# Kernel optimization log

Measured on AMD Instinct MI355X. Metric: run time of the kernel, lower is better.

## Reference

```python
import jax, jax.numpy as jnp
import numpy as np

# Config from module init / global Args
H = 8        # n_head
DK = 64      # d_k
DV = 64      # d_v
D = 512      # d_model
KSZ = 3      # kernel_size (args.kernel_size)
B_PARAM = 0.001
CUR_HEAD = 3
ALPHA_C = -float(np.log(B_PARAM / (H - 1) * CUR_HEAD))  # alpha_c (nonzero head)
EPS = 1e-6


def setup_inputs() -> dict:
    key = jax.random.key(0)
    ks = jax.random.split(key, 8)
    B, L = 2, 2048
    q = jax.random.normal(ks[0], (B, L, D), jnp.float32)
    k = jax.random.normal(ks[1], (B, L, D), jnp.float32)
    v = jax.random.normal(ks[2], (B, L, D), jnp.float32)
    # Linear weights stored torch-style: [out_features, in_features]
    w_q = jax.random.normal(ks[3], (H * DK, D), jnp.float32) * 0.02
    w_k = jax.random.normal(ks[4], (H * DK, D), jnp.float32) * 0.02
    w_v = jax.random.normal(ks[5], (H * DV, D), jnp.float32) * 0.02
    w_fc = jax.random.normal(ks[6], (D, H * DV), jnp.float32) * 0.02
    gamma = jnp.ones((D,), jnp.float32)
    beta = jnp.zeros((D,), jnp.float32)
    return {"q": q, "k": k, "v": v, "w_q": w_q, "w_k": w_k, "w_v": w_v,
            "w_fc": w_fc, "gamma": gamma, "beta": beta}


def reference(q, k, v, w_q, w_k, w_v, w_fc, gamma, beta):
    B, L, _ = q.shape
    residual = q
    # QKV projections -> [B, H, L, d]
    qh = jnp.einsum('bld,ed->ble', q, w_q).reshape(B, L, H, DK).transpose(0, 2, 1, 3)
    kh = jnp.einsum('bld,ed->ble', k, w_k).reshape(B, L, H, DK).transpose(0, 2, 1, 3)
    vh = jnp.einsum('bld,ed->ble', v, w_v).reshape(B, L, H, DV).transpose(0, 2, 1, 3)
    # Scores: matmul(q / sqrt(d_k), k^T)  (LaSAttention receives d_k = d_k**0.5)
    attn = jnp.einsum('bhqd,bhkd->bhqk', qh, kh) / jnp.sqrt(jnp.float32(DK))
    # Distance weighting: eld = alpha_c * -(x - y) * attn, d_l[i,j] = j - i
    idx = jnp.arange(L)
    d_l = idx[None, :] - idx[:, None]                      # [L, L]
    eld_mat = (-ALPHA_C * d_l).astype(attn.dtype)
    eld = eld_mat[None, None, :, :] * attn
    # Softmax then avg_pool1d(kernel=KSZ, stride=1, pad=(KSZ-1)//2, count_include_pad)
    p = jax.nn.softmax(eld, axis=-1)                       # [B, H, L, L]
    pad = (KSZ - 1) // 2
    pp = jnp.pad(p, ((0, 0), (0, 0), (0, 0), (pad, pad)))
    pooled = sum(pp[..., j:j + L] for j in range(KSZ)) / jnp.float32(KSZ)
    # Value matmul (seq lengths equal so no trimming needed)
    out = jnp.einsum('bhqk,bhkd->bhqd', pooled, vh)
    out = out.transpose(0, 2, 1, 3).reshape(B, L, H * DV)
    # Output projection (dropout is identity in eval), residual, LayerNorm
    out = jnp.einsum('ble,de->bld', out, w_fc)
    out = out[:, :, None, :] + residual[:, :, None, :]     # [B, L, 1, D]
    mu = out.mean(axis=-1, keepdims=True)
    var = ((out - mu) ** 2).mean(axis=-1, keepdims=True)
    out = (out - mu) / jnp.sqrt(var + EPS) * gamma + beta
    return (out, pooled)
```

## Files before the change

kernel.cpp:

```cpp
#include <hip/hip_runtime.h>
#include <cstddef>
#include <cstdint>

#define ALPHA_C 7.7550531393693407f
constexpr int BB = 2;
constexpr int LL = 2048;
constexpr int HH = 8;
constexpr size_t OUT0  = (size_t)BB * LL * 512;
constexpr size_t PLANE = (size_t)BB * HH * LL * 64;
constexpr size_t XN    = (size_t)BB * LL * 512;
constexpr size_t WN    = (size_t)512 * 512;

typedef __attribute__((ext_vector_type(8))) short bf16x8;
typedef __attribute__((ext_vector_type(4))) short short4v;
typedef __attribute__((ext_vector_type(4))) float f32x4;

__device__ inline short f2bf(float x) {
  union { float f; unsigned u; } un; un.f = x;
  unsigned r = un.u + 0x7fffu + ((un.u >> 16) & 1u);
  return (short)(r >> 16);
}
__device__ inline float bf2f(short s) {
  union { unsigned u; float f; } un; un.u = ((unsigned)(unsigned short)s) << 16;
  return un.f;
}
__device__ inline void split3(float x, short& h, short& m, short& l) {
  h = f2bf(x); float r = x - bf2f(h);
  m = f2bf(r); float r2 = r - bf2f(m);
  l = f2bf(r2);
}

__global__ __launch_bounds__(256) void k_split3x(
    const float* __restrict__ a, const float* __restrict__ b, const float* __restrict__ c,
    short* __restrict__ da, short* __restrict__ db, short* __restrict__ dc, size_t n)
{
  size_t i = ((size_t)blockIdx.x * 256 + threadIdx.x) * 4;
  if (i >= n) return;
  const float* srcs[3] = {a, b, c};
  short* dsts[3] = {da, db, dc};
  #pragma unroll
  for (int s = 0; s < 3; ++s) {
    float4 x = *(const float4*)&srcs[s][i];
    short4v h, m, l;
    short th, tm, tl;
    split3(x.x, th, tm, tl); h[0] = th; m[0] = tm; l[0] = tl;
    split3(x.y, th, tm, tl); h[1] = th; m[1] = tm; l[1] = tl;
    split3(x.z, th, tm, tl); h[2] = th; m[2] = tm; l[2] = tl;
    split3(x.w, th, tm, tl); h[3] = th; m[3] = tm; l[3] = tl;
    *(short4v*)&dsts[s][i]         = h;
    *(short4v*)&dsts[s][n + i]     = m;
    *(short4v*)&dsts[s][2 * n + i] = l;
  }
}

__global__ __launch_bounds__(256) void k_cvtbf(
    const float* __restrict__ src, short* __restrict__ dst, size_t n)
{
  size_t i = ((size_t)blockIdx.x * 256 + threadIdx.x) * 8;
  if (i >= n) return;
  float4 a = *(const float4*)&src[i];
  float4 b = *(const float4*)&src[i + 4];
  bf16x8 o;
  o[0] = f2bf(a.x); o[1] = f2bf(a.y); o[2] = f2bf(a.z); o[3] = f2bf(a.w);
  o[4] = f2bf(b.x); o[5] = f2bf(b.y); o[6] = f2bf(b.z); o[7] = f2bf(b.w);
  *(bf16x8*)&dst[i] = o;
}

__global__ __launch_bounds__(256) void k_vavg(
    const short* __restrict__ vt, short* __restrict__ vavgt)
{
  const size_t row = blockIdx.x;
  const short* src = vt + row * LL;
  short* dst = vavgt + row * LL;
  const int c0 = threadIdx.x * 8;
  bf16x8 x = *(const bf16x8*)&src[c0];
  float xf[10];
  xf[0] = (c0 > 0) ? bf2f(src[c0 - 1]) : 0.f;
  #pragma unroll
  for (int i = 0; i < 8; ++i) xf[i + 1] = bf2f(x[i]);
  xf[9] = (c0 + 8 < LL) ? bf2f(src[c0 + 8]) : 0.f;
  bf16x8 o;
  #pragma unroll
  for (int i = 0; i < 8; ++i) o[i] = f2bf((xf[i] + xf[i + 1] + xf[i + 2]) * (1.0f / 3.0f));
  *(bf16x8*)&dst[c0] = o;
}

__global__ __launch_bounds__(256) void k_proj(
    const short* __restrict__ xq, const short* __restrict__ xk, const short* __restrict__ xv,
    const short* __restrict__ wq3, const short* __restrict__ wk3, const short* __restrict__ wv3,
    short* __restrict__ qs, short* __restrict__ ks, short* __restrict__ vt)
{
  const int bx  = blockIdx.x;
  const int sel = bx >> 3;
  const int n0  = (bx & 7) * 64;
  const int m0  = blockIdx.y * 64;
  const short* X = sel == 0 ? xq  : (sel == 1 ? xk  : xv);
  const short* W = sel == 0 ? wq3 : (sel == 1 ? wk3 : wv3);

  __shared__ short Xs[3][64 * 72];
  __shared__ short Ws[3][64 * 72];
  const int tid = threadIdx.x;
  const int lane = tid & 63, w = tid >> 6;
  const int quad = lane >> 4, l15 = lane & 15, colg = l15;
  const int sr8 = tid >> 3, sc8 = (tid & 7) * 8;

  f32x4 acc[4];
  #pragma unroll
  for (int t = 0; t < 4; ++t) { acc[t][0]=0.f; acc[t][1]=0.f; acc[t][2]=0.f; acc[t][3]=0.f; }

  for (int kt = 0; kt < 8; ++kt) {
    const int k0 = kt * 64;
    #pragma unroll
    for (int p = 0; p < 3; ++p) {
      #pragma unroll
      for (int it = 0; it < 2; ++it) {
        int r = it * 32 + sr8;
        *(bf16x8*)&Xs[p][r * 72 + sc8] = *(const bf16x8*)&X[p * XN + (size_t)(m0 + r) * 512 + k0 + sc8];
        *(bf16x8*)&Ws[p][r * 72 + sc8] = *(const bf16x8*)&W[p * WN + (size_t)(n0 + r) * 512 + k0 + sc8];
      }
    }
    __syncthreads();
    #pragma unroll
    for (int ch = 0; ch < 2; ++ch) {
      const int ka = (quad << 3) + ch * 32;
      const int ar = (w * 16 + l15) * 72 + ka;
      bf16x8 ah = *(const bf16x8*)&Xs[0][ar];
      bf16x8 am = *(const bf16x8*)&Xs[1][ar];
      bf16x8 al = *(const bf16x8*)&Xs[2][ar];
      #pragma unroll
      for (int t = 0; t < 4; ++t) {
        const int br = (t * 16 + l15) * 72 + ka;
        bf16x8 bh_ = *(const bf16x8*)&Ws[0][br];
        bf16x8 bm_ = *(const bf16x8*)&Ws[1][br];
        bf16x8 bl_ = *(const bf16x8*)&Ws[2][br];
        acc[t] = __builtin_amdgcn_mfma_f32_16x16x32_bf16(ah, bh_, acc[t], 0, 0, 0);
        acc[t] = __builtin_amdgcn_mfma_f32_16x16x32_bf16(ah, bm_, acc[t], 0, 0, 0);
        acc[t] = __builtin_amdgcn_mfma_f32_16x16x32_bf16(am, bh_, acc[t], 0, 0, 0);
        acc[t] = __builtin_amdgcn_mfma_f32_16x16x32_bf16(ah, bl_, acc[t], 0, 0, 0);
        acc[t] = __builtin_amdgcn_mfma_f32_16x16x32_bf16(al, bh_, acc[t], 0, 0, 0);
        acc[t] = __builtin_amdgcn_mfma_f32_16x16x32_bf16(am, bm_, acc[t], 0, 0, 0);
      }
    }
    __syncthreads();
  }

  if (sel < 2) {
    short* Y = sel == 0 ? qs : ks;
    #pragma unroll
    for (int t = 0; t < 4; ++t) {
      const int e = n0 + t * 16 + colg, h = e >> 6, dk = e & 63;
      #pragma unroll
      for (int r = 0; r < 4; ++r) {
        const int m = m0 + w * 16 + quad * 4 + r;
        const int b = m >> 11, l = m & 2047;
        size_t base = ((size_t)(b * HH + h) * LL + l) * 64 + dk;
        short hh, mm, ll; split3(acc[t][r], hh, mm, ll);
        Y[base] = hh; Y[PLANE + base] = mm; Y[2 * PLANE + base] = ll;
      }
    }
  } else {
    const int b  = m0 >> 11;
    const int l0 = (m0 & 2047) + w * 16 + quad * 4;
    #pragma unroll
    for (int t = 0; t < 4; ++t) {
      const int e = n0 + t * 16 + colg, h = e >> 6, dk = e & 63;
      short4v s;
      #pragma unroll
      for (int r = 0; r < 4; ++r) s[r] = f2bf(acc[t][r]);
      *(short4v*)&vt[(((size_t)b * HH + h) * 64 + dk) * LL + l0] = s;
    }
  }
}

__global__ __launch_bounds__(256) void k_stats(
    const short* __restrict__ qs, const short* __restrict__ ks,
    float* __restrict__ statspart)
{
  const int i0 = blockIdx.x * 64;
  const int jh = blockIdx.y;
  const int bh = blockIdx.z;
  __shared__ short Ks[3][64 * 72];
  const int tid = threadIdx.x;
  const int lane = tid & 63, w = tid >> 6;
  const int quad = lane >> 4, colg = lane & 15, l15 = lane & 15;
  const int sr8 = tid >> 3, sc8 = (tid & 7) * 8;

  bf16x8 qf[3][2];
  {
    const size_t qoff = ((size_t)bh * LL + i0 + w * 16 + l15) * 64 + (quad << 3);
    #pragma unroll
    for (int p = 0; p < 3; ++p)
      #pragma unroll
      for (int ch = 0; ch < 2; ++ch)
        qf[p][ch] = *(const bf16x8*)&qs[p * PLANE + qoff + ch * 32];
  }

  const int jt0 = jh * 16;
  const short* kbase = ks + (size_t)bh * LL * 64;
  #pragma unroll
  for (int p = 0; p < 3; ++p)
    #pragma unroll
    for (int it = 0; it < 2; ++it) {
      int r = it * 32 + sr8;
      *(bf16x8*)&Ks[p][r * 72 + sc8] =
          *(const bf16x8*)&kbase[p * PLANE + ((size_t)jt0 * 64 + r) * 64 + sc8];
    }
  __syncthreads();

  float M[4], S[4];
  #pragma unroll
  for (int r = 0; r < 4; ++r) { M[r] = -3.0e38f; S[r] = 0.f; }

  for (int jj = 0; jj < 16; ++jj) {
    const int jt = jt0 + jj;
    const int j0 = jt * 64;
    bf16x8 kreg[3][2];
    if (jj + 1 < 16) {
      #pragma unroll
      for (int p = 0; p < 3; ++p)
        #pragma unroll
        for (int it = 0; it < 2; ++it) {
          int r = it * 32 + sr8;
          kreg[p][it] = *(const bf16x8*)&kbase[p * PLANE + ((size_t)(jt + 1) * 64 + r) * 64 + sc8];
        }
    }

    f32x4 acc[4];
    #pragma unroll
    for (int t = 0; t < 4; ++t) { acc[t][0]=0.f; acc[t][1]=0.f; acc[t][2]=0.f; acc[t][3]=0.f; }
    #pragma unroll
    for (int ch = 0; ch < 2; ++ch) {
      const int ka = (quad << 3) + ch * 32;
      #pragma unroll
      for (int t = 0; t < 4; ++t) {
        const int br = (t * 16 + l15) * 72 + ka;
        bf16x8 bh_ = *(const bf16x8*)&Ks[0][br];
        bf16x8 bm_ = *(const bf16x8*)&Ks[1][br];
        bf16x8 bl_ = *(const bf16x8*)&Ks[2][br];
        acc[t] = __builtin_amdgcn_mfma_f32_16x16x32_bf16(qf[0][ch], bh_, acc[t], 0, 0, 0);
        acc[t] = __builtin_amdgcn_mfma_f32_16x16x32_bf16(qf[0][ch], bm_, acc[t], 0, 0, 0);
        acc[t] = __builtin_amdgcn_mfma_f32_16x16x32_bf16(qf[1][ch], bh_, acc[t], 0, 0, 0);
        acc[t] = __builtin_amdgcn_mfma_f32_16x16x32_bf16(qf[0][ch], bl_, acc[t], 0, 0, 0);
        acc[t] = __builtin_amdgcn_mfma_f32_16x16x32_bf16(qf[2][ch], bh_, acc[t], 0, 0, 0);
        acc[t] = __builtin_amdgcn_mfma_f32_16x16x32_bf16(qf[1][ch], bm_, acc[t], 0, 0, 0);
      }
    }

    #pragma unroll
    for (int r = 0; r < 4; ++r) {
      const int irow = i0 + w * 16 + quad * 4 + r;
      float e0 = -ALPHA_C * (float)(j0 +  0 + colg - irow) * (acc[0][r] * 0.125f);
      float e1 = -ALPHA_C * (float)(j0 + 16 + colg - irow) * (acc[1][r] * 0.125f);
      float e2 = -ALPHA_C * (float)(j0 + 32 + colg - irow) * (acc[2][r] * 0.125f);
      float e3 = -ALPHA_C * (float)(j0 + 48 + colg - irow) * (acc[3][r] * 0.125f);
      float mx = fmaxf(fmaxf(e0, e1), fmaxf(e2, e3));
      float nM = fmaxf(M[r], mx);
      S[r] = S[r] * __expf(M[r] - nM)
           + __expf(e0 - nM) + __expf(e1 - nM) + __expf(e2 - nM) + __expf(e3 - nM);
      M[r] = nM;
    }

    __syncthreads();
    if (jj + 1 < 16) {
      #pragma unroll
      for (int p = 0; p < 3; ++p)
        #pragma unroll
        for (int it = 0; it < 2; ++it) {
          int r = it * 32 + sr8;
          *(bf16x8*)&Ks[p][r * 72 + sc8] = kreg[p][it];
        }
    }
    __syncthreads();
  }

  #pragma unroll
  for (int r = 0; r < 4; ++r) {
    float M_ = M[r], S_ = S[r];
    #pragma unroll
    for (int d = 1; d < 16; d <<= 1) {
      float Mo = __shfl_xor(M_, d);
      float So = __shfl_xor(S_, d);
      float nM = fmaxf(M_, Mo);
      S_ = S_ * __expf(M_ - nM) + So * __expf(Mo - nM);
      M_ = nM;
    }
    if (colg == 0) {
      int irow = i0 + w * 16 + quad * 4 + r;
      size_t idx = (((size_t)jh * 16 + bh) * LL + irow) * 2;
      statspart[idx] = M_; statspart[idx + 1] = S_;
    }
  }
}

__global__ __launch_bounds__(256) void k_mergestats(
    const float* __restrict__ statspart, float* __restrict__ rowstats)
{
  const size_t row = (size_t)blockIdx.x * 256 + threadIdx.x;
  float2 a = *(const float2*)&statspart[row * 2];
  float2 b = *(const float2*)&statspart[(size_t)16 * LL * 2 + row * 2];
  float nM = fmaxf(a.x, b.x);
  float S = a.y * __expf(a.x - nM) + b.y * __expf(b.x - nM);
  rowstats[row * 2] = nM; rowstats[row * 2 + 1] = S;
}

__global__ __launch_bounds__(256) void k_pool_pv(
    const short* __restrict__ qs, const short* __restrict__ ks,
    const short* __restrict__ vavgt, const float* __restrict__ rowstats,
    float* __restrict__ pooled, short* __restrict__ outh)
{
  const int i0 = blockIdx.x * 64;
  const int bh = blockIdx.y;
  const int b = bh >> 3, h = bh & 7;
  float*       Pg = pooled + (size_t)bh * LL * LL;
  const short* Vt = vavgt + (size_t)bh * 64 * LL;
  const short* kbase = ks + (size_t)bh * LL * 64;

  __shared__ short Ks[3][64 * 72];
  __shared__ short Vsm[64 * 72];
  __shared__ short Pa[2][64 * 72];
  __shared__ float Mrow[64], invSr[64], lhalo[64];

  const int tid = threadIdx.x;
  const int lane = tid & 63, w = tid >> 6;
  const int quad = lane >> 4, colg = lane & 15, l15 = lane & 15;
  const int sr8 = tid >> 3, sc8 = (tid & 7) * 8;

  bf16x8 qf[3][2];
  {
    const size_t qoff = ((size_t)bh * LL + i0 + w * 16 + l15) * 64 + (quad << 3);
    #pragma unroll
    for (int p = 0; p < 3; ++p)
      #pragma unroll
      for (int ch = 0; ch < 2; ++ch)
        qf[p][ch] = *(const bf16x8*)&qs[p * PLANE + qoff + ch * 32];
  }
  if (tid < 64) {
    float2 ms = *(const float2*)&rowstats[((size_t)bh * LL + i0 + tid) * 2];
    Mrow[tid] = ms.x; invSr[tid] = 1.0f / ms.y; lhalo[tid] = 0.f;
  }

  #pragma unroll
  for (int p = 0; p < 3; ++p)
    #pragma unroll
    for (int it = 0; it < 2; ++it) {
      int r = it * 32 + sr8;
      *(bf16x8*)&Ks[p][r * 72 + sc8] = *(const bf16x8*)&kbase[p * PLANE + (size_t)r * 64 + sc8];
    }
  __syncthreads();

  f32x4 pv[4];
  #pragma unroll
  for (int t = 0; t < 4; ++t) { pv[t][0]=0.f; pv[t][1]=0.f; pv[t][2]=0.f; pv[t][3]=0.f; }

  for (int jt = 0; jt <= 32; ++jt) {
    if (jt < 32) {
      const int j0 = jt * 64;
      f32x4 acc[4];
      #pragma unroll
      for (int t = 0; t < 4; ++t) { acc[t][0]=0.f; acc[t][1]=0.f; acc[t][2]=0.f; acc[t][3]=0.f; }
      #pragma unroll
      for (int ch = 0; ch < 2; ++ch) {
        const int ka = (quad << 3) + ch * 32;
        #pragma unroll
        for (int t = 0; t < 4; ++t) {
          const int br = (t * 16 + l15) * 72 + ka;
          bf16x8 bh_ = *(const bf16x8*)&Ks[0][br];
          bf16x8 bm_ = *(const bf16x8*)&Ks[1][br];
          bf16x8 bl_ = *(const bf16x8*)&Ks[2][br];
          acc[t] = __builtin_amdgcn_mfma_f32_16x16x32_bf16(qf[0][ch], bh_, acc[t], 0, 0, 0);
          acc[t] = __builtin_amdgcn_mfma_f32_16x16x32_bf16(qf[0][ch], bm_, acc[t], 0, 0, 0);
          acc[t] = __builtin_amdgcn_mfma_f32_16x16x32_bf16(qf[1][ch], bh_, acc[t], 0, 0, 0);
          acc[t] = __builtin_amdgcn_mfma_f32_16x16x32_bf16(qf[0][ch], bl_, acc[t], 0, 0, 0);
          acc[t] = __builtin_amdgcn_mfma_f32_16x16x32_bf16(qf[2][ch], bh_, acc[t], 0, 0, 0);
          acc[t] = __builtin_amdgcn_mfma_f32_16x16x32_bf16(qf[1][ch], bm_, acc[t], 0, 0, 0);
        }
      }
      short* Pc = Pa[jt & 1];
      #pragma unroll
      for (int r = 0; r < 4; ++r) {
        const int row = w * 16 + quad * 4 + r;
        const int irow = i0 + row;
        const float Mr = Mrow[row], iS = invSr[row];
        #pragma unroll
        for (int t = 0; t < 4; ++t) {
          int jl = t * 16 + colg;
          float e = -ALPHA_C * (float)(j0 + jl - irow) * (acc[t][r] * 0.125f);
          Pc[row * 72 + jl] = f2bf(__expf(e - Mr) * iS);
        }
      }
    }
    if (jt >= 1) {
      #pragma unroll
      for (int it = 0; it < 2; ++it) {
        int d = it * 32 + sr8;
        *(bf16x8*)&Vsm[d * 72 + sc8] = *(const bf16x8*)&Vt[(size_t)d * LL + (jt - 1) * 64 + sc8];
      }
    }
    __syncthreads();

    if (jt >= 1) {
      const short* Pp = Pa[(jt - 1) & 1];
      const short* Pn = Pa[jt & 1];
      #pragma unroll
      for (int u = 0; u < 2; ++u) {
        const int row = (u == 0) ? (tid >> 3) : (tid >> 3) + 32;
        const int c0 = (tid & 7) * 8;
        bf16x8 x = *(const bf16x8*)&Pp[row * 72 + c0];
        float xf[8];
        #pragma unroll
        for (int i = 0; i < 8; ++i) xf[i] = bf2f(x[i]);
        float lft = (c0 == 0)  ? lhalo[row] : bf2f(Pp[row * 72 + c0 - 1]);
        float rgt = (c0 == 56) ? ((jt < 32) ? bf2f(Pn[row * 72]) : 0.f)
                               : bf2f(Pp[row * 72 + c0 + 8]);
        f32x4 o0, o1;
        o0[0] = (lft   + xf[0] + xf[1]) * (1.0f/3.0f);
        o0[1] = (xf[0] + xf[1] + xf[2]) * (1.0f/3.0f);
        o0[2] = (xf[1] + xf[2] + xf[3]) * (1.0f/3.0f);
        o0[3] = (xf[2] + xf[3] + xf[4]) * (1.0f/3.0f);
        o1[0] = (xf[3] + xf[4] + xf[5]) * (1.0f/3.0f);
        o1[1] = (xf[4] + xf[5] + xf[6]) * (1.0f/3.0f);
        o1[2] = (xf[5] + xf[6] + xf[7]) * (1.0f/3.0f);
        o1[3] = (xf[6] + xf[7] + rgt  ) * (1.0f/3.0f);
        float* dst = &Pg[(size_t)(i0 + row) * LL + (jt - 1) * 64 + c0];
        __builtin_nontemporal_store(o0, (f32x4*)dst);
        __builtin_nontemporal_store(o1, (f32x4*)(dst + 4));
        if (c0 == 56) lhalo[row] = xf[7];
      }
      #pragma unroll
      for (int ch = 0; ch < 2; ++ch) {
        const int ka = (quad << 3) + ch * 32;
        bf16x8 af = *(const bf16x8*)&Pp[(w * 16 + l15) * 72 + ka];
        #pragma unroll
        for (int t = 0; t < 4; ++t) {
          bf16x8 bfv = *(const bf16x8*)&Vsm[(t * 16 + l15) * 72 + ka];
          pv[t] = __builtin_amdgcn_mfma_f32_16x16x32_bf16(af, bfv, pv[t], 0, 0, 0);
        }
      }
    }
    if (jt + 1 < 32) {
      #pragma unroll
      for (int p = 0; p < 3; ++p)
        #pragma unroll
        for (int it = 0; it < 2; ++it) {
          int r = it * 32 + sr8;
          *(bf16x8*)&Ks[p][r * 72 + sc8] =
              *(const bf16x8*)&kbase[p * PLANE + ((size_t)(jt + 1) * 64 + r) * 64 + sc8];
        }
    }
    __syncthreads();
  }

  #pragma unroll
  for (int t = 0; t < 4; ++t)
    #pragma unroll
    for (int r = 0; r < 4; ++r) {
      int i = i0 + w * 16 + quad * 4 + r;
      int d = t * 16 + colg;
      outh[((size_t)b * LL + i) * 512 + h * 64 + d] = f2bf(pv[t][r]);
    }
}

__global__ __launch_bounds__(256) void k_fc(
    const short* __restrict__ outh, const short* __restrict__ wfcb, float* __restrict__ fcout)
{
  const int n0 = blockIdx.x * 64;
  const int m0 = blockIdx.y * 64;
  __shared__ short Asm[64 * 72];
  __shared__ short Bsm[64 * 72];
  const int tid = threadIdx.x;
  const int lane = tid & 63, w = tid >> 6;
  const int sr8 = tid >> 3, sc8 = (tid & 7) * 8;

  f32x4 acc[4];
  #pragma unroll
  for (int t = 0; t < 4; ++t) { acc[t][0]=0.f; acc[t][1]=0.f; acc[t][2]=0.f; acc[t][3]=0.f; }

  for (int k0 = 0; k0 < 512; k0 += 64) {
    #pragma unroll
    for (int it = 0; it < 2; ++it) {
      int r = it * 32 + sr8;
      *(bf16x8*)&Asm[r * 72 + sc8] = *(const bf16x8*)&outh[(size_t)(m0 + r) * 512 + k0 + sc8];
      *(bf16x8*)&Bsm[r * 72 + sc8] = *(const bf16x8*)&wfcb[(size_t)(n0 + r) * 512 + k0 + sc8];
    }
    __syncthreads();
    #pragma unroll
    for (int ch = 0; ch < 2; ++ch) {
      const int ka = ((lane >> 4) << 3) + ch * 32;
      bf16x8 af = *(const bf16x8*)&Asm[(w * 16 + (lane & 15)) * 72 + ka];
      #pragma unroll
      for (int t = 0; t < 4; ++t) {
        bf16x8 bfv = *(const bf16x8*)&Bsm[(t * 16 + (lane & 15)) * 72 + ka];
        acc[t] = __builtin_amdgcn_mfma_f32_16x16x32_bf16(af, bfv, acc[t], 0, 0, 0);
      }
    }
    __syncthreads();
  }
  const int q4 = lane >> 4, colg = lane & 15;
  #pragma unroll
  for (int t = 0; t < 4; ++t)
    #pragma unroll
    for (int r = 0; r < 4; ++r) {
      int m = m0 + w * 16 + q4 * 4 + r;
      fcout[(size_t)m * 512 + n0 + t * 16 + colg] = acc[t][r];
    }
}

__global__ __launch_bounds__(256) void k_ln(
    const float* __restrict__ fcout, const float* __restrict__ resid,
    const float* __restrict__ gamma, const float* __restrict__ beta,
    float* __restrict__ out)
{
  const size_t row = blockIdx.x;
  const int tid = threadIdx.x;
  __shared__ float red[256];

  float x0 = fcout[row * 512 + tid]       + resid[row * 512 + tid];
  float x1 = fcout[row * 512 + 256 + tid] + resid[row * 512 + 256 + tid];

  red[tid] = x0 + x1; __syncthreads();
  for (int off = 128; off > 0; off >>= 1) {
    if (tid < off) red[tid] += red[tid + off];
    __syncthreads();
  }
  const float mu = red[0] * (1.0f / 512.0f); __syncthreads();

  float d0 = x0 - mu, d1 = x1 - mu;
  red[tid] = d0 * d0 + d1 * d1; __syncthreads();
  for (int off = 128; off > 0; off >>= 1) {
    if (tid < off) red[tid] += red[tid + off];
    __syncthreads();
  }
  const float var = red[0] * (1.0f / 512.0f);
  const float rstd = 1.0f / sqrtf(var + 1e-6f);

  out[row * 512 + tid]       = d0 * rstd * gamma[tid]       + beta[tid];
  out[row * 512 + 256 + tid] = d1 * rstd * gamma[tid + 256] + beta[tid + 256];
}

extern "C" void kernel_launch(void* const* d_in, const int* in_sizes, int n_in,
                              void* d_out, int out_size, void* d_ws, size_t ws_size,
                              hipStream_t stream)
{
  const float* q     = (const float*)d_in[0];
  const float* k     = (const float*)d_in[1];
  const float* v     = (const float*)d_in[2];
  const float* wq    = (const float*)d_in[3];
  const float* wk    = (const float*)d_in[4];
  const float* wv    = (const float*)d_in[5];
  const float* wfc   = (const float*)d_in[6];
  const float* gamma = (const float*)d_in[7];
  const float* beta  = (const float*)d_in[8];

  float* out    = (float*)d_out;
  float* pooled = out + OUT0;

  short* xq    = (short*)d_ws;
  short* xk    = xq + 3 * XN;
  short* xv    = xk + 3 * XN;
  short* wq3   = xv + 3 * XN;
  short* wk3   = wq3 + 3 * WN;
  short* wv3   = wk3 + 3 * WN;
  short* qsp   = wv3 + 3 * WN;
  short* ksp   = qsp + 3 * PLANE;
  short* vt    = ksp + 3 * PLANE;
  short* vavgt = vt + PLANE;
  short* wfcb  = vavgt + PLANE;
  short* outh  = wfcb + WN;
  float* statspart = (float*)(outh + OUT0);
  float* rowstats  = statspart + 4 * (size_t)BB * HH * LL;
  float* fcout     = rowstats + 2 * (size_t)BB * HH * LL;

  k_split3x<<<dim3((unsigned)(XN / 4 / 256)), 256, 0, stream>>>(q, k, v, xq, xk, xv, XN);
  k_split3x<<<dim3((unsigned)(WN / 4 / 256)), 256, 0, stream>>>(wq, wk, wv, wq3, wk3, wv3, WN);
  k_cvtbf  <<<dim3((unsigned)(WN / 8 / 256)), 256, 0, stream>>>(wfc, wfcb, WN);
  k_proj   <<<dim3(24, 64), 256, 0, stream>>>(xq, xk, xv, wq3, wk3, wv3, qsp, ksp, vt);
  k_vavg   <<<dim3(1024),   256, 0, stream>>>(vt, vavgt);
  k_stats  <<<dim3(32, 2, 16), 256, 0, stream>>>(qsp, ksp, statspart);
  k_mergestats<<<dim3(128), 256, 0, stream>>>(statspart, rowstats);
  k_pool_pv<<<dim3(32, 16), 256, 0, stream>>>(qsp, ksp, vavgt, rowstats, pooled, outh);
  k_fc     <<<dim3(8, 64),  256, 0, stream>>>(outh, wfcb, fcout);
  k_ln     <<<dim3(4096),   256, 0, stream>>>(fcout, q, gamma, beta, out);
}
```

Measured before the change: 496.7 us.

## Fold softmax constants into exp2 form and prefetch K/V tiles into registers

Rewrites the score-to-exponent math to use base-2 exponentials, with alpha, the 1/sqrt(dk) scale and log2(e) folded into one constant. The distance factor is now built incrementally per row. In the pool/PV kernel, the normalization becomes a single fma with a per-row log-sum constant held in registers, replacing shared-memory row stats and a multiply by the reciprocal sum. Next K and V tiles are loaded into registers at the top of each iteration so global latency overlaps the MFMA work, at the cost of extra register pressure.

```diff
diff --git a/kernel.cpp b/kernel.cpp
--- a/kernel.cpp
+++ b/kernel.cpp
@@ -10,6 +10,9 @@
 constexpr size_t PLANE = (size_t)BB * HH * LL * 64;
 constexpr size_t XN    = (size_t)BB * LL * 512;
 constexpr size_t WN    = (size_t)512 * 512;
+
+constexpr float AL2N   = (float)(-7.7550531393693407 * 0.125 * 1.4426950408889634);
+constexpr float AL2N16 = AL2N * 16.0f;
 
 typedef __attribute__((ext_vector_type(8))) short bf16x8;
 typedef __attribute__((ext_vector_type(4))) short short4v;
@@ -207,13 +210,14 @@
     }
   __syncthreads();
 
-  float M[4], S[4];
-  #pragma unroll
-  for (int r = 0; r < 4; ++r) { M[r] = -3.0e38f; S[r] = 0.f; }
+  float M[4], S[4], fb0[4];
+  #pragma unroll
+  for (int r = 0; r < 4; ++r) {
+    M[r] = -3.0e38f; S[r] = 0.f;
+    fb0[r] = (float)(jt0 * 64 + colg - (i0 + w * 16 + quad * 4 + r));
+  }
 
   for (int jj = 0; jj < 16; ++jj) {
-    const int jt = jt0 + jj;
-    const int j0 = jt * 64;
     bf16x8 kreg[3][2];
     if (jj + 1 < 16) {
       #pragma unroll
@@ -221,7 +225,7 @@
         #pragma unroll
         for (int it = 0; it < 2; ++it) {
           int r = it * 32 + sr8;
-          kreg[p][it] = *(const bf16x8*)&kbase[p * PLANE + ((size_t)(jt + 1) * 64 + r) * 64 + sc8];
+          kreg[p][it] = *(const bf16x8*)&kbase[p * PLANE + ((size_t)(jt0 + jj + 1) * 64 + r) * 64 + sc8];
         }
     }
 
@@ -248,16 +252,20 @@
 
     #pragma unroll
     for (int r = 0; r < 4; ++r) {
-      const int irow = i0 + w * 16 + quad * 4 + r;
-      float e0 = -ALPHA_C * (float)(j0 +  0 + colg - irow) * (acc[0][r] * 0.125f);
-      float e1 = -ALPHA_C * (float)(j0 + 16 + colg - irow) * (acc[1][r] * 0.125f);
-      float e2 = -ALPHA_C * (float)(j0 + 32 + colg - irow) * (acc[2][r] * 0.125f);
-      float e3 = -ALPHA_C * (float)(j0 + 48 + colg - irow) * (acc[3][r] * 0.125f);
+      float pe0 = AL2N * fb0[r];
+      float pe1 = pe0 + AL2N16;
+      float pe2 = pe1 + AL2N16;
+      float pe3 = pe2 + AL2N16;
+      float e0 = pe0 * acc[0][r];
+      float e1 = pe1 * acc[1][r];
+      float e2 = pe2 * acc[2][r];
+      float e3 = pe3 * acc[3][r];
       float mx = fmaxf(fmaxf(e0, e1), fmaxf(e2, e3));
       float nM = fmaxf(M[r], mx);
-      S[r] = S[r] * __expf(M[r] - nM)
-           + __expf(e0 - nM) + __expf(e1 - nM) + __expf(e2 - nM) + __expf(e3 - nM);
+      S[r] = S[r] * exp2f(M[r] - nM)
+           + exp2f(e0 - nM) + exp2f(e1 - nM) + exp2f(e2 - nM) + exp2f(e3 - nM);
       M[r] = nM;
+      fb0[r] += 64.0f;
     }
 
     __syncthreads();
@@ -281,7 +289,7 @@
       float Mo = __shfl_xor(M_, d);
       float So = __shfl_xor(S_, d);
       float nM = fmaxf(M_, Mo);
-      S_ = S_ * __expf(M_ - nM) + So * __expf(Mo - nM);
+      S_ = S_ * exp2f(M_ - nM) + So * exp2f(Mo - nM);
       M_ = nM;
     }
     if (colg == 0) {
@@ -299,7 +307,7 @@
   float2 a = *(const float2*)&statspart[row * 2];
   float2 b = *(const float2*)&statspart[(size_t)16 * LL * 2 + row * 2];
   float nM = fmaxf(a.x, b.x);
-  float S = a.y * __expf(a.x - nM) + b.y * __expf(b.x - nM);
+  float S = a.y * exp2f(a.x - nM) + b.y * exp2f(b.x - nM);
   rowstats[row * 2] = nM; rowstats[row * 2 + 1] = S;
 }
 
@@ -318,7 +326,7 @@
   __shared__ short Ks[3][64 * 72];
   __shared__ short Vsm[64 * 72];
   __shared__ short Pa[2][64 * 72];
-  __shared__ float Mrow[64], invSr[64], lhalo[64];
+  __shared__ float lhalo[64];
 
   const int tid = threadIdx.x;
   const int lane = tid & 63, w = tid >> 6;
@@ -334,10 +342,15 @@
       for (int ch = 0; ch < 2; ++ch)
         qf[p][ch] = *(const bf16x8*)&qs[p * PLANE + qoff + ch * 32];
   }
-  if (tid < 64) {
-    float2 ms = *(const float2*)&rowstats[((size_t)bh * LL + i0 + tid) * 2];
-    Mrow[tid] = ms.x; invSr[tid] = 1.0f / ms.y; lhalo[tid] = 0.f;
-  }
+  float nC2[4], fb0[4];
+  #pragma unroll
+  for (int r = 0; r < 4; ++r) {
+    const int irow = i0 + w * 16 + quad * 4 + r;
+    float2 ms = *(const float2*)&rowstats[((size_t)bh * LL + irow) * 2];
+    nC2[r] = -(ms.x + log2f(ms.y));
+    fb0[r] = (float)(colg - irow);
+  }
+  if (tid < 64) lhalo[tid] = 0.f;
 
   #pragma unroll
   for (int p = 0; p < 3; ++p)
@@ -353,8 +366,25 @@
   for (int t = 0; t < 4; ++t) { pv[t][0]=0.f; pv[t][1]=0.f; pv[t][2]=0.f; pv[t][3]=0.f; }
 
   for (int jt = 0; jt <= 32; ++jt) {
+    bf16x8 kreg[3][2];
+    if (jt + 1 < 32) {
+      #pragma unroll
+      for (int p = 0; p < 3; ++p)
+        #pragma unroll
+        for (int it = 0; it < 2; ++it) {
+          int r = it * 32 + sr8;
+          kreg[p][it] = *(const bf16x8*)&kbase[p * PLANE + ((size_t)(jt + 1) * 64 + r) * 64 + sc8];
+        }
+    }
+    bf16x8 vreg[2];
+    if (jt >= 1) {
+      #pragma unroll
+      for (int it = 0; it < 2; ++it) {
+        int d = it * 32 + sr8;
+        vreg[it] = *(const bf16x8*)&Vt[(size_t)d * LL + (jt - 1) * 64 + sc8];
+      }
+    }
     if (jt < 32) {
-      const int j0 = jt * 64;
       f32x4 acc[4];
       #pragma unroll
       for (int t = 0; t < 4; ++t) { acc[t][0]=0.f; acc[t][1]=0.f; acc[t][2]=0.f; acc[t][3]=0.f; }
@@ -379,21 +409,22 @@
       #pragma unroll
       for (int r = 0; r < 4; ++r) {
         const int row = w * 16 + quad * 4 + r;
-        const int irow = i0 + row;
-        const float Mr = Mrow[row], iS = invSr[row];
-        #pragma unroll
-        for (int t = 0; t < 4; ++t) {
-          int jl = t * 16 + colg;
-          float e = -ALPHA_C * (float)(j0 + jl - irow) * (acc[t][r] * 0.125f);
-          Pc[row * 72 + jl] = f2bf(__expf(e - Mr) * iS);
-        }
+        float pe0 = AL2N * fb0[r];
+        float pe1 = pe0 + AL2N16;
+        float pe2 = pe1 + AL2N16;
+        float pe3 = pe2 + AL2N16;
+        Pc[row * 72 +      colg] = f2bf(exp2f(fmaf(pe0, acc[0][r], nC2[r])));
+        Pc[row * 72 + 16 + colg] = f2bf(exp2f(fmaf(pe1, acc[1][r], nC2[r])));
+        Pc[row * 72 + 32 + colg] = f2bf(exp2f(fmaf(pe2, acc[2][r], nC2[r])));
+        Pc[row * 72 + 48 + colg] = f2bf(exp2f(fmaf(pe3, acc[3][r], nC2[r])));
+        fb0[r] += 64.0f;
       }
     }
     if (jt >= 1) {
       #pragma unroll
       for (int it = 0; it < 2; ++it) {
         int d = it * 32 + sr8;
-        *(bf16x8*)&Vsm[d * 72 + sc8] = *(const bf16x8*)&Vt[(size_t)d * LL + (jt - 1) * 64 + sc8];
+        *(bf16x8*)&Vsm[d * 72 + sc8] = vreg[it];
       }
     }
     __syncthreads();
@@ -429,7 +460,7 @@
       #pragma unroll
       for (int ch = 0; ch < 2; ++ch) {
         const int ka = (quad << 3) + ch * 32;
-        bf16x8 af = *(const bf16x8*)&Pp[(w * 16 + l15) * 72 + ka];
+        bf16x8 af = *(const bf16x8*)&Pa[(jt - 1) & 1][(w * 16 + l15) * 72 + ka];
         #pragma unroll
         for (int t = 0; t < 4; ++t) {
           bf16x8 bfv = *(const bf16x8*)&Vsm[(t * 16 + l15) * 72 + ka];
@@ -443,8 +474,7 @@
         #pragma unroll
         for (int it = 0; it < 2; ++it) {
           int r = it * 32 + sr8;
-          *(bf16x8*)&Ks[p][r * 72 + sc8] =
-              *(const bf16x8*)&kbase[p * PLANE + ((size_t)(jt + 1) * 64 + r) * 64 + sc8];
+          *(bf16x8*)&Ks[p][r * 72 + sc8] = kreg[p][it];
         }
     }
     __syncthreads();
```

After: 504.2 us. About the same (+1.5%).
